# Optimization experiments

Measured on AMD Instinct MI355X. Metric: run time of the kernel, lower is better.

## Reference

```python
import jax, jax.numpy as jnp
import numpy as np

LLM_DIM = 4096
VOCAB = 4096
HEADS = 8
INNER = 512
HEAD_DIM = INNER // HEADS
T = 8192


def setup_inputs() -> dict:
    key = jax.random.key(0)
    ks = jax.random.split(key, 6)
    s = 0.02
    return {
        "token_input": jax.random.normal(ks[0], (T, LLM_DIM), dtype=jnp.float32),
        "learned_queries": jax.random.normal(ks[1], (VOCAB, INNER), dtype=jnp.float32),
        "w_q": jax.random.normal(ks[2], (INNER, INNER), dtype=jnp.float32) * s,
        "w_k": jax.random.normal(ks[3], (LLM_DIM, INNER), dtype=jnp.float32) * s,
        "w_v": jax.random.normal(ks[4], (LLM_DIM, INNER), dtype=jnp.float32) * s,
        "w_out": jax.random.normal(ks[5], (INNER, LLM_DIM), dtype=jnp.float32) * s,
    }


def reference(token_input, learned_queries, w_q, w_k, w_v, w_out):
    scale = HEAD_DIM ** -0.5
    # projections (Linear with no bias): x @ W  (W stored as [in, out])
    q = learned_queries @ w_q            # [V, inner]
    k = token_input @ w_k                # [T, inner]
    v = token_input @ w_v                # [T, inner]
    q = q.reshape(VOCAB, HEADS, HEAD_DIM)
    k = k.reshape(T, HEADS, HEAD_DIM)
    v = v.reshape(T, HEADS, HEAD_DIM)
    # scores [H, V, T]
    attn = jnp.einsum('vhd,thd->hvt', q, k) * scale
    attn = jax.nn.softmax(attn, axis=-1)
    out = jnp.einsum('hvt,thd->vhd', attn, v).reshape(VOCAB, INNER)
    return out @ w_out                   # [V, llm_dim]
```

## Files before the change

kernel.cpp:

```cpp
#include <hip/hip_runtime.h>
#include <hip/hip_bf16.h>

typedef unsigned short u16;
typedef unsigned int u32;
typedef __bf16 bf16x8 __attribute__((ext_vector_type(8)));
typedef float f32x4 __attribute__((ext_vector_type(4)));
typedef u32 u32x4 __attribute__((ext_vector_type(4)));

#define LLM_DIM 4096
#define VOCAB   4096
#define HEADS   8
#define INNER   512
#define TOK     8192
#define KVSTR   1024

__device__ __forceinline__ u16 f2bf(float f){
  u32 u = __builtin_bit_cast(u32, f);
  u += 0x7FFFu + ((u >> 16) & 1u);
  return (u16)(u >> 16);
}

__device__ __forceinline__ void async16(u16* lds, const u16* g){
  __builtin_amdgcn_global_load_lds((const __attribute__((address_space(1))) u32*)g,
                                   (__attribute__((address_space(3))) u32*)lds, 16, 0, 0);
}

__global__ void cast_kernel(const float* __restrict__ in, u16* __restrict__ out, int n4){
  int stride = gridDim.x * blockDim.x;
  for (int i = blockIdx.x*blockDim.x + threadIdx.x; i < n4; i += stride){
    float4 v = ((const float4*)in)[i];
    ushort4 o;
    o.x = f2bf(v.x); o.y = f2bf(v.y); o.z = f2bf(v.z); o.w = f2bf(v.w);
    ((ushort4*)out)[i] = o;
  }
}

__global__ void transpose_cast_kernel(const float* __restrict__ in, u16* __restrict__ out, int R, int C){
  __shared__ float tile[32][33];
  int tilesPerRow = C >> 5;
  int bx = blockIdx.x % tilesPerRow, by = blockIdx.x / tilesPerRow;
  int tx = threadIdx.x & 31, ty = threadIdx.x >> 5;
  int r0 = by << 5, c0 = bx << 5;
  #pragma unroll
  for (int k = 0; k < 4; ++k) tile[ty + 8*k][tx] = in[(size_t)(r0 + ty + 8*k)*C + c0 + tx];
  __syncthreads();
  #pragma unroll
  for (int k = 0; k < 4; ++k) out[(size_t)(c0 + ty + 8*k)*R + r0 + tx] = f2bf(tile[tx][ty + 8*k]);
}

__global__ void transpose_bf_kernel(const u16* __restrict__ in, u16* __restrict__ out, int R, int C, int istride){
  __shared__ u16 tile[32][33];
  int tilesPerRow = C >> 5;
  int bx = blockIdx.x % tilesPerRow, by = blockIdx.x / tilesPerRow;
  int tx = threadIdx.x & 31, ty = threadIdx.x >> 5;
  int r0 = by << 5, c0 = bx << 5;
  #pragma unroll
  for (int k = 0; k < 4; ++k) tile[ty + 8*k][tx] = in[(size_t)(r0 + ty + 8*k)*istride + c0 + tx];
  __syncthreads();
  #pragma unroll
  for (int k = 0; k < 4; ++k) out[(size_t)(c0 + ty + 8*k)*R + r0 + tx] = tile[tx][ty + 8*k];
}

template<bool CF32>
__global__ __launch_bounds__(256) void gemm_bt(const u16* __restrict__ A, const u16* __restrict__ BT,
                                               void* __restrict__ Cp, int M, int N, int K){
  __shared__ __align__(16) u16 As[128*32];
  __shared__ __align__(16) u16 Bs[128*32];
  const int m0 = blockIdx.x * 128, n0 = blockIdx.y * 128;
  const int t = threadIdx.x;
  const int lane = t & 63, w = t >> 6;
  const int wm = (w & 1) * 64, wn = (w >> 1) * 64;
  const int lr = lane & 15, lg = lane >> 4;
  f32x4 acc[4][4] = {};
  const int srow = t >> 2, scx = t & 3;
  const u16* ga = A  + (size_t)(m0 + srow)*K + scx*8;
  const u16* gb = BT + (size_t)(n0 + srow)*K + scx*8;
  const int nk = K >> 5;
  for (int kt = 0; kt < nk; ++kt){
    async16(As + t*8,        ga);
    async16(As + (256+t)*8,  ga + (size_t)64*K);
    async16(Bs + t*8,        gb);
    async16(Bs + (256+t)*8,  gb + (size_t)64*K);
    ga += 32; gb += 32;
    __syncthreads();
    bf16x8 a[4], b[4];
    #pragma unroll
    for (int m = 0; m < 4; ++m) a[m] = *(const bf16x8*)(As + (wm + m*16 + lr)*32 + lg*8);
    #pragma unroll
    for (int n = 0; n < 4; ++n) b[n] = *(const bf16x8*)(Bs + (wn + n*16 + lr)*32 + lg*8);
    #pragma unroll
    for (int m = 0; m < 4; ++m)
      #pragma unroll
      for (int n = 0; n < 4; ++n)
        acc[m][n] = __builtin_amdgcn_mfma_f32_16x16x32_bf16(a[m], b[n], acc[m][n], 0, 0, 0);
    __syncthreads();
  }
  #pragma unroll
  for (int m = 0; m < 4; ++m)
    #pragma unroll
    for (int n = 0; n < 4; ++n)
      #pragma unroll
      for (int r = 0; r < 4; ++r){
        int row = m0 + wm + m*16 + lg*4 + r;
        int col = n0 + wn + n*16 + lr;
        if constexpr (CF32) ((float*)Cp)[(size_t)row*N + col] = acc[m][n][r];
        else                ((u16*)Cp)[(size_t)row*N + col]   = f2bf(acc[m][n][r]);
      }
}

template<int GG, bool PART>
__global__ __launch_bounds__(256, 2) void flash_kernel(const u16* __restrict__ Q, const u16* __restrict__ Kg,
                                                       const u16* __restrict__ VT,
                                                       float* __restrict__ Og, float* __restrict__ Rg,
                                                       u16* __restrict__ Oout){
  __shared__ __align__(16) u16 Ks[64*64];
  __shared__ __align__(16) u16 Vs[64*64];
  const int qt = blockIdx.x, h = blockIdx.y, g = blockIdx.z;
  const int t = threadIdx.x, lane = t & 63, w = t >> 6;
  const int lr = lane & 15, lg = lane >> 4, swz = lr & 7;
  const int bq = qt*256 + w*64;
  bf16x8 qfr[4][2];
  #pragma unroll
  for (int qf = 0; qf < 4; ++qf)
    #pragma unroll
    for (int hf = 0; hf < 2; ++hf)
      qfr[qf][hf] = *(const bf16x8*)(Q + (size_t)(bq + qf*16 + lr)*INNER + h*64 + hf*32 + lg*8);
  f32x4 o[4][4] = {};
  float rsum[4] = {0.f, 0.f, 0.f, 0.f};
  const float sc = 0.125f * 1.44269504088896340736f;
  const int srow = t >> 3;
  const int scol = ((t & 7) ^ (srow & 7)) * 8;
  const u16* gk = Kg + (size_t)srow*KVSTR + h*64 + scol;
  const u16* gv = VT + (size_t)(h*64 + srow)*TOK + scol;
  const int tbase0 = g * (TOK/GG);
  for (int tt = 0; tt < TOK/GG/64; ++tt){
    const int tb = tbase0 + tt*64;
    async16(Ks + t*8,       gk + (size_t)tb*KVSTR);
    async16(Ks + (256+t)*8, gk + (size_t)(tb+32)*KVSTR);
    async16(Vs + t*8,       gv + tb);
    async16(Vs + (256+t)*8, gv + (size_t)32*TOK + tb);
    __syncthreads();
    bf16x8 kf[4][2], vf[4][2];
    #pragma unroll
    for (int ct = 0; ct < 4; ++ct)
      #pragma unroll
      for (int hf = 0; hf < 2; ++hf)
        kf[ct][hf] = *(const bf16x8*)(Ks + (ct*16 + lr)*64 + ((hf*4 + lg) ^ swz)*8);
    #pragma unroll
    for (int dt = 0; dt < 4; ++dt)
      #pragma unroll
      for (int f2 = 0; f2 < 2; ++f2)
        vf[dt][f2] = *(const bf16x8*)(Vs + (dt*16 + lr)*64 + ((f2*4 + lg) ^ swz)*8);
    #pragma unroll
    for (int qf = 0; qf < 4; ++qf){
      f32x4 s[4] = {};
      #pragma unroll
      for (int ct = 0; ct < 4; ++ct){
        s[ct] = __builtin_amdgcn_mfma_f32_16x16x32_bf16(kf[ct][0], qfr[qf][0], s[ct], 0, 0, 0);
        s[ct] = __builtin_amdgcn_mfma_f32_16x16x32_bf16(kf[ct][1], qfr[qf][1], s[ct], 0, 0, 0);
      }
      u32 wds[4][2];
      #pragma unroll
      for (int ct = 0; ct < 4; ++ct)
        #pragma unroll
        for (int hh = 0; hh < 2; ++hh){
          float p0 = exp2f(s[ct][2*hh]   * sc);
          float p1 = exp2f(s[ct][2*hh+1] * sc);
          rsum[qf] += p0 + p1;
          wds[ct][hh] = (u32)f2bf(p0) | ((u32)f2bf(p1) << 16);
        }
      #pragma unroll
      for (int f2 = 0; f2 < 2; ++f2){
        u32 pw[4];
        #pragma unroll
        for (int k = 0; k < 4; ++k){
          int srcl = lr + 16*(2*(lg & 1) + (k >> 1));
          u32 a = (u32)__shfl((int)wds[2*f2][k & 1],     srcl, 64);
          u32 b = (u32)__shfl((int)wds[2*f2 + 1][k & 1], srcl, 64);
          pw[k] = (lg < 2) ? a : b;
        }
        u32x4 pwv = {pw[0], pw[1], pw[2], pw[3]};
        bf16x8 pf = __builtin_bit_cast(bf16x8, pwv);
        #pragma unroll
        for (int dt = 0; dt < 4; ++dt)
          o[qf][dt] = __builtin_amdgcn_mfma_f32_16x16x32_bf16(pf, vf[dt][f2], o[qf][dt], 0, 0, 0);
      }
    }
    __syncthreads();
  }
  #pragma unroll
  for (int qf = 0; qf < 4; ++qf){
    float r0 = rsum[qf];
    r0 += __shfl_xor(r0, 16, 64);
    r0 += __shfl_xor(r0, 32, 64);
    if constexpr (PART){
      if (lg == 0) Rg[((size_t)g*HEADS + h)*VOCAB + bq + qf*16 + lr] = r0;
      #pragma unroll
      for (int dt = 0; dt < 4; ++dt)
        #pragma unroll
        for (int r = 0; r < 4; ++r)
          Og[(size_t)g*VOCAB*INNER + (size_t)(bq + qf*16 + lg*4 + r)*INNER + h*64 + dt*16 + lr] = o[qf][dt][r];
    } else {
      float invv[4];
      #pragma unroll
      for (int r = 0; r < 4; ++r) invv[r] = 1.0f / __shfl(r0, lg*4 + r, 64);
      #pragma unroll
      for (int dt = 0; dt < 4; ++dt)
        #pragma unroll
        for (int r = 0; r < 4; ++r)
          Oout[(size_t)(bq + qf*16 + lg*4 + r)*INNER + h*64 + dt*16 + lr] = f2bf(o[qf][dt][r] * invv[r]);
    }
  }
}

__global__ void combine_kernel(const float* __restrict__ Og, const float* __restrict__ Rg,
                               u16* __restrict__ out, int G){
  int idx = blockIdx.x*blockDim.x + threadIdx.x;
  int q = idx >> 7, d4 = idx & 127;
  int h = d4 >> 4;
  float4 acc = make_float4(0.f, 0.f, 0.f, 0.f);
  float rs = 0.f;
  for (int g = 0; g < G; ++g){
    float4 v = ((const float4*)(Og + (size_t)g*VOCAB*INNER))[idx];
    acc.x += v.x; acc.y += v.y; acc.z += v.z; acc.w += v.w;
    rs += Rg[((size_t)g*HEADS + h)*VOCAB + q];
  }
  float inv = 1.0f / rs;
  ushort4 r;
  r.x = f2bf(acc.x * inv); r.y = f2bf(acc.y * inv);
  r.z = f2bf(acc.z * inv); r.w = f2bf(acc.w * inv);
  ((ushort4*)out)[idx] = r;
}

extern "C" void kernel_launch(void* const* d_in, const int* in_sizes, int n_in,
                              void* d_out, int out_size, void* d_ws, size_t ws_size,
                              hipStream_t stream){
  const float* tok = (const float*)d_in[0];
  const float* lq  = (const float*)d_in[1];
  const float* wq  = (const float*)d_in[2];
  const float* wk  = (const float*)d_in[3];
  const float* wv  = (const float*)d_in[4];
  const float* wo  = (const float*)d_in[5];

  constexpr int G = 4;
  u16* p = (u16*)d_ws;
  u16* tokbf = p; p += (size_t)TOK*LLM_DIM;
  u16* lqbf  = p; p += (size_t)VOCAB*INNER;
  u16* wqT   = p; p += (size_t)INNER*INNER;
  u16* wkvT  = p; p += (size_t)KVSTR*LLM_DIM;
  u16* woT   = p; p += (size_t)LLM_DIM*INNER;
  u16* kv    = p; p += (size_t)TOK*KVSTR;
  u16* qbf   = p; p += (size_t)VOCAB*INNER;
  u16* vt    = p; p += (size_t)INNER*TOK;
  u16* aout  = p; p += (size_t)VOCAB*INNER;
  float* Rg  = (float*)p; p += (size_t)G*HEADS*VOCAB*2;
  size_t used = (size_t)((u16*)p - (u16*)d_ws) * 2;
  float* Og  = (float*)tokbf;
  bool partial_ok = (ws_size >= used);

  cast_kernel<<<2048, 256, 0, stream>>>(tok, tokbf, TOK*LLM_DIM/4);
  cast_kernel<<<512, 256, 0, stream>>>(lq, lqbf, VOCAB*INNER/4);
  transpose_cast_kernel<<<(INNER/32)*(INNER/32),   256, 0, stream>>>(wq, wqT, INNER, INNER);
  transpose_cast_kernel<<<(INNER/32)*(LLM_DIM/32), 256, 0, stream>>>(wk, wkvT, LLM_DIM, INNER);
  transpose_cast_kernel<<<(INNER/32)*(LLM_DIM/32), 256, 0, stream>>>(wv, wkvT + (size_t)INNER*LLM_DIM, LLM_DIM, INNER);
  transpose_cast_kernel<<<(LLM_DIM/32)*(INNER/32), 256, 0, stream>>>(wo, woT, INNER, LLM_DIM);

  gemm_bt<false><<<dim3(TOK/128, KVSTR/128), 256, 0, stream>>>(tokbf, wkvT, kv, TOK, KVSTR, LLM_DIM);
  gemm_bt<false><<<dim3(VOCAB/128, INNER/128), 256, 0, stream>>>(lqbf, wqT, qbf, VOCAB, INNER, INNER);

  transpose_bf_kernel<<<(INNER/32)*(TOK/32), 256, 0, stream>>>(kv + INNER, vt, TOK, INNER, KVSTR);

  if (partial_ok){
    flash_kernel<G, true><<<dim3(VOCAB/256, HEADS, G), 256, 0, stream>>>(qbf, kv, vt, Og, Rg, nullptr);
    combine_kernel<<<(VOCAB*INNER/4)/256, 256, 0, stream>>>(Og, Rg, aout, G);
  } else {
    flash_kernel<1, false><<<dim3(VOCAB/256, HEADS, 1), 256, 0, stream>>>(qbf, kv, vt, nullptr, nullptr, aout);
  }

  gemm_bt<true><<<dim3(VOCAB/128, LLM_DIM/128), 256, 0, stream>>>(aout, woT, d_out, VOCAB, LLM_DIM, INNER);
}
```

Baseline: 546.0 us.

## Switch flash attention to 32x32x16 MFMA with permlane swaps and prescaled Q

The attention kernel moves from 16x16x32 to 32x32x16 bf16 MFMA tiles, which reorganises the Q, K and V fragment layouts and the output accumulators. The P matrix is re-laid out with v_permlane32_swap instead of the __shfl-based exchange, and the softmax probabilities are packed with the hardware v_cvt_pk_bf16_f32 and the raw exp2 intrinsic. The softmax scale and log2e factor are folded into the Q projection GEMM epilogue, which removes a per-score multiply. The aim is fewer MFMA issues, cheaper lane exchanges and lighter exp and convert work. The cost is more rounding in Q, higher register pressure, and a denormalization loop that now does a shuffle and a divide for every output element.

```diff
diff --git a/kernel.cpp b/kernel.cpp
--- a/kernel.cpp
+++ b/kernel.cpp
@@ -5,6 +5,7 @@
 typedef unsigned int u32;
 typedef __bf16 bf16x8 __attribute__((ext_vector_type(8)));
 typedef float f32x4 __attribute__((ext_vector_type(4)));
+typedef float f32x16 __attribute__((ext_vector_type(16)));
 typedef u32 u32x4 __attribute__((ext_vector_type(4)));
 
 #define LLM_DIM 4096
@@ -63,7 +64,7 @@
 
 template<bool CF32>
 __global__ __launch_bounds__(256) void gemm_bt(const u16* __restrict__ A, const u16* __restrict__ BT,
-                                               void* __restrict__ Cp, int M, int N, int K){
+                                               void* __restrict__ Cp, int M, int N, int K, float scale){
   __shared__ __align__(16) u16 As[128*32];
   __shared__ __align__(16) u16 Bs[128*32];
   const int m0 = blockIdx.x * 128, n0 = blockIdx.y * 128;
@@ -104,7 +105,7 @@
         int row = m0 + wm + m*16 + lg*4 + r;
         int col = n0 + wn + n*16 + lr;
         if constexpr (CF32) ((float*)Cp)[(size_t)row*N + col] = acc[m][n][r];
-        else                ((u16*)Cp)[(size_t)row*N + col]   = f2bf(acc[m][n][r]);
+        else                ((u16*)Cp)[(size_t)row*N + col]   = f2bf(acc[m][n][r] * scale);
       }
 }
 
@@ -117,17 +118,16 @@
   __shared__ __align__(16) u16 Vs[64*64];
   const int qt = blockIdx.x, h = blockIdx.y, g = blockIdx.z;
   const int t = threadIdx.x, lane = t & 63, w = t >> 6;
-  const int lr = lane & 15, lg = lane >> 4, swz = lr & 7;
+  const int l31 = lane & 31, hi = lane >> 5, sw7 = l31 & 7;
   const int bq = qt*256 + w*64;
-  bf16x8 qfr[4][2];
-  #pragma unroll
-  for (int qf = 0; qf < 4; ++qf)
-    #pragma unroll
-    for (int hf = 0; hf < 2; ++hf)
-      qfr[qf][hf] = *(const bf16x8*)(Q + (size_t)(bq + qf*16 + lr)*INNER + h*64 + hf*32 + lg*8);
-  f32x4 o[4][4] = {};
-  float rsum[4] = {0.f, 0.f, 0.f, 0.f};
-  const float sc = 0.125f * 1.44269504088896340736f;
+  bf16x8 qfr[2][4];
+  #pragma unroll
+  for (int qf = 0; qf < 2; ++qf)
+    #pragma unroll
+    for (int win = 0; win < 4; ++win)
+      qfr[qf][win] = *(const bf16x8*)(Q + (size_t)(bq + qf*32 + l31)*INNER + h*64 + win*16 + hi*8);
+  f32x16 o[2][2] = {};
+  float rsum[2] = {0.f, 0.f};
   const int srow = t >> 3;
   const int scol = ((t & 7) ^ (srow & 7)) * 8;
   const u16* gk = Kg + (size_t)srow*KVSTR + h*64 + scol;
@@ -140,75 +140,72 @@
     async16(Vs + t*8,       gv + tb);
     async16(Vs + (256+t)*8, gv + (size_t)32*TOK + tb);
     __syncthreads();
-    bf16x8 kf[4][2], vf[4][2];
-    #pragma unroll
-    for (int ct = 0; ct < 4; ++ct)
-      #pragma unroll
-      for (int hf = 0; hf < 2; ++hf)
-        kf[ct][hf] = *(const bf16x8*)(Ks + (ct*16 + lr)*64 + ((hf*4 + lg) ^ swz)*8);
-    #pragma unroll
-    for (int dt = 0; dt < 4; ++dt)
-      #pragma unroll
-      for (int f2 = 0; f2 < 2; ++f2)
-        vf[dt][f2] = *(const bf16x8*)(Vs + (dt*16 + lr)*64 + ((f2*4 + lg) ^ swz)*8);
-    #pragma unroll
-    for (int qf = 0; qf < 4; ++qf){
-      f32x4 s[4] = {};
-      #pragma unroll
-      for (int ct = 0; ct < 4; ++ct){
-        s[ct] = __builtin_amdgcn_mfma_f32_16x16x32_bf16(kf[ct][0], qfr[qf][0], s[ct], 0, 0, 0);
-        s[ct] = __builtin_amdgcn_mfma_f32_16x16x32_bf16(kf[ct][1], qfr[qf][1], s[ct], 0, 0, 0);
-      }
-      u32 wds[4][2];
-      #pragma unroll
-      for (int ct = 0; ct < 4; ++ct)
-        #pragma unroll
-        for (int hh = 0; hh < 2; ++hh){
-          float p0 = exp2f(s[ct][2*hh]   * sc);
-          float p1 = exp2f(s[ct][2*hh+1] * sc);
-          rsum[qf] += p0 + p1;
-          wds[ct][hh] = (u32)f2bf(p0) | ((u32)f2bf(p1) << 16);
-        }
-      #pragma unroll
-      for (int f2 = 0; f2 < 2; ++f2){
-        u32 pw[4];
-        #pragma unroll
-        for (int k = 0; k < 4; ++k){
-          int srcl = lr + 16*(2*(lg & 1) + (k >> 1));
-          u32 a = (u32)__shfl((int)wds[2*f2][k & 1],     srcl, 64);
-          u32 b = (u32)__shfl((int)wds[2*f2 + 1][k & 1], srcl, 64);
-          pw[k] = (lg < 2) ? a : b;
-        }
-        u32x4 pwv = {pw[0], pw[1], pw[2], pw[3]};
-        bf16x8 pf = __builtin_bit_cast(bf16x8, pwv);
-        #pragma unroll
-        for (int dt = 0; dt < 4; ++dt)
-          o[qf][dt] = __builtin_amdgcn_mfma_f32_16x16x32_bf16(pf, vf[dt][f2], o[qf][dt], 0, 0, 0);
+    bf16x8 vf[2][4];
+    #pragma unroll
+    for (int dt = 0; dt < 2; ++dt)
+      #pragma unroll
+      for (int tw = 0; tw < 4; ++tw)
+        vf[dt][tw] = *(const bf16x8*)(Vs + (dt*32 + l31)*64 + (((tw*2 + hi) ^ sw7))*8);
+    #pragma unroll
+    for (int ts = 0; ts < 2; ++ts){
+      bf16x8 kf[4];
+      #pragma unroll
+      for (int win = 0; win < 4; ++win)
+        kf[win] = *(const bf16x8*)(Ks + (ts*32 + l31)*64 + (((win*2 + hi) ^ sw7))*8);
+      #pragma unroll
+      for (int qf = 0; qf < 2; ++qf){
+        f32x16 s = {};
+        #pragma unroll
+        for (int win = 0; win < 4; ++win)
+          s = __builtin_amdgcn_mfma_f32_32x32x16_bf16(kf[win], qfr[qf][win], s, 0, 0, 0);
+        u32 qw[4][2];
+        #pragma unroll
+        for (int c = 0; c < 4; ++c){
+          float p0 = __builtin_amdgcn_exp2f(s[4*c+0]);
+          float p1 = __builtin_amdgcn_exp2f(s[4*c+1]);
+          float p2 = __builtin_amdgcn_exp2f(s[4*c+2]);
+          float p3 = __builtin_amdgcn_exp2f(s[4*c+3]);
+          rsum[qf] += (p0 + p1) + (p2 + p3);
+          asm("v_cvt_pk_bf16_f32 %0, %1, %2" : "=v"(qw[c][0]) : "v"(p0), "v"(p1));
+          asm("v_cvt_pk_bf16_f32 %0, %1, %2" : "=v"(qw[c][1]) : "v"(p2), "v"(p3));
+        }
+        #pragma unroll
+        for (int kw = 0; kw < 2; ++kw){
+          u32 a0 = qw[2*kw][0], b0 = qw[2*kw+1][0];
+          u32 a1 = qw[2*kw][1], b1 = qw[2*kw+1][1];
+          asm("v_permlane32_swap_b32 %0, %1" : "+v"(a0), "+v"(b0));
+          asm("v_permlane32_swap_b32 %0, %1" : "+v"(a1), "+v"(b1));
+          u32x4 pwv = {a0, a1, b0, b1};
+          bf16x8 pf = __builtin_bit_cast(bf16x8, pwv);
+          #pragma unroll
+          for (int dt = 0; dt < 2; ++dt)
+            o[qf][dt] = __builtin_amdgcn_mfma_f32_32x32x16_bf16(pf, vf[dt][ts*2 + kw], o[qf][dt], 0, 0, 0);
+        }
       }
     }
     __syncthreads();
   }
   #pragma unroll
-  for (int qf = 0; qf < 4; ++qf){
-    float r0 = rsum[qf];
-    r0 += __shfl_xor(r0, 16, 64);
-    r0 += __shfl_xor(r0, 32, 64);
+  for (int qf = 0; qf < 2; ++qf){
+    float rt = rsum[qf] + __shfl_xor(rsum[qf], 32, 64);
     if constexpr (PART){
-      if (lg == 0) Rg[((size_t)g*HEADS + h)*VOCAB + bq + qf*16 + lr] = r0;
-      #pragma unroll
-      for (int dt = 0; dt < 4; ++dt)
-        #pragma unroll
-        for (int r = 0; r < 4; ++r)
-          Og[(size_t)g*VOCAB*INNER + (size_t)(bq + qf*16 + lg*4 + r)*INNER + h*64 + dt*16 + lr] = o[qf][dt][r];
+      if (hi == 0) Rg[((size_t)g*HEADS + h)*VOCAB + bq + qf*32 + l31] = rt;
+      #pragma unroll
+      for (int dt = 0; dt < 2; ++dt)
+        #pragma unroll
+        for (int r = 0; r < 16; ++r){
+          int ql = (r & 3) + 8*(r >> 2) + 4*hi;
+          Og[(size_t)g*VOCAB*INNER + (size_t)(bq + qf*32 + ql)*INNER + h*64 + dt*32 + l31] = o[qf][dt][r];
+        }
     } else {
-      float invv[4];
-      #pragma unroll
-      for (int r = 0; r < 4; ++r) invv[r] = 1.0f / __shfl(r0, lg*4 + r, 64);
-      #pragma unroll
-      for (int dt = 0; dt < 4; ++dt)
-        #pragma unroll
-        for (int r = 0; r < 4; ++r)
-          Oout[(size_t)(bq + qf*16 + lg*4 + r)*INNER + h*64 + dt*16 + lr] = f2bf(o[qf][dt][r] * invv[r]);
+      #pragma unroll
+      for (int dt = 0; dt < 2; ++dt)
+        #pragma unroll
+        for (int r = 0; r < 16; ++r){
+          int ql = (r & 3) + 8*(r >> 2) + 4*hi;
+          float inv = 1.0f / __shfl(rt, ql, 64);
+          Oout[(size_t)(bq + qf*32 + ql)*INNER + h*64 + dt*32 + l31] = f2bf(o[qf][dt][r] * inv);
+        }
     }
   }
 }
@@ -243,6 +240,7 @@
   const float* wo  = (const float*)d_in[5];
 
   constexpr int G = 4;
+  const float QSC = 0.125f * 1.44269504088896340736f;
   u16* p = (u16*)d_ws;
   u16* tokbf = p; p += (size_t)TOK*LLM_DIM;
   u16* lqbf  = p; p += (size_t)VOCAB*INNER;
@@ -265,8 +263,8 @@
   transpose_cast_kernel<<<(INNER/32)*(LLM_DIM/32), 256, 0, stream>>>(wv, wkvT + (size_t)INNER*LLM_DIM, LLM_DIM, INNER);
   transpose_cast_kernel<<<(LLM_DIM/32)*(INNER/32), 256, 0, stream>>>(wo, woT, INNER, LLM_DIM);
 
-  gemm_bt<false><<<dim3(TOK/128, KVSTR/128), 256, 0, stream>>>(tokbf, wkvT, kv, TOK, KVSTR, LLM_DIM);
-  gemm_bt<false><<<dim3(VOCAB/128, INNER/128), 256, 0, stream>>>(lqbf, wqT, qbf, VOCAB, INNER, INNER);
+  gemm_bt<false><<<dim3(TOK/128, KVSTR/128), 256, 0, stream>>>(tokbf, wkvT, kv, TOK, KVSTR, LLM_DIM, 1.0f);
+  gemm_bt<false><<<dim3(VOCAB/128, INNER/128), 256, 0, stream>>>(lqbf, wqT, qbf, VOCAB, INNER, INNER, QSC);
 
   transpose_bf_kernel<<<(INNER/32)*(TOK/32), 256, 0, stream>>>(kv + INNER, vt, TOK, INNER, KVSTR);
 
@@ -277,5 +275,5 @@
     flash_kernel<1, false><<<dim3(VOCAB/256, HEADS, 1), 256, 0, stream>>>(qbf, kv, vt, nullptr, nullptr, aout);
   }
 
-  gemm_bt<true><<<dim3(VOCAB/128, LLM_DIM/128), 256, 0, stream>>>(aout, woT, d_out, VOCAB, LLM_DIM, INNER);
-}
+  gemm_bt<true><<<dim3(VOCAB/128, LLM_DIM/128), 256, 0, stream>>>(aout, woT, d_out, VOCAB, LLM_DIM, INNER, 1.0f);
+}
```

New measurement: 471.6 us. -13.6%, faster.
